# Optimization experiments

Hardware: AMD Instinct MI355X
Metric: run time of the kernel (lower is better)

Reference implementation:

```python
import jax, jax.numpy as jnp
import numpy as np

N_NODES = 50000
N_EDGES = 800000
IN_CH = 64
OUT_CH = 32
HEADS = 4
NUM_EDGE_TYPES = 64


def _sincos_pe(max_len, d_model):
    pos = np.arange(max_len, dtype=np.float32)[:, None]
    div = np.exp(np.arange(0, d_model, 2, dtype=np.float32) * (-np.log(10000.0) / d_model))
    pe = np.zeros((max_len, d_model), dtype=np.float32)
    pe[:, 0::2] = np.sin(pos * div)
    pe[:, 1::2] = np.cos(pos * div)
    return jnp.asarray(pe)


def setup_inputs() -> dict:
    key = jax.random.key(0)
    k1, k2, k3, k4, k5, k6 = jax.random.split(key, 6)
    x = jax.random.uniform(k1, (N_NODES, IN_CH), dtype=jnp.float32)
    edge_index = jax.random.randint(k2, (2, N_EDGES), 0, N_NODES, dtype=jnp.int64)
    edge_type = jax.random.randint(k3, (N_EDGES,), 0, NUM_EDGE_TYPES, dtype=jnp.int64)
    pe = _sincos_pe(NUM_EDGE_TYPES, IN_CH)
    W = jax.random.normal(k4, (IN_CH, HEADS * OUT_CH), dtype=jnp.float32) * 0.1
    att_src = jax.random.normal(k5, (HEADS, OUT_CH), dtype=jnp.float32) * 0.1
    att_dst = jax.random.normal(k6, (HEADS, OUT_CH), dtype=jnp.float32) * 0.1
    bias = jnp.zeros((HEADS * OUT_CH,), dtype=jnp.float32)
    return {"x": x, "edge_index": edge_index, "edge_type": edge_type, "pe": pe,
            "W": W, "att_src": att_src, "att_dst": att_dst, "bias": bias}


def reference(x, edge_index, edge_type, pe, W, att_src, att_dst, bias):
    N = x.shape[0]
    H, C = att_src.shape
    src, dst = edge_index[0], edge_index[1]

    # edge-wise positional encoding scatter-added into source nodes
    x_pos = x.at[src].add(pe[edge_type])

    # GATConv (PyG defaults: add_self_loops=True, negative_slope=0.2, concat=True)
    xl = (x_pos @ W).reshape(N, H, C)              # [N, H, C]
    a_src = (xl * att_src[None]).sum(-1)           # [N, H]
    a_dst = (xl * att_dst[None]).sum(-1)           # [N, H]

    self_idx = jnp.arange(N)
    src2 = jnp.concatenate([src, self_idx])        # [E'] with self loops
    dst2 = jnp.concatenate([dst, self_idx])

    alpha = jax.nn.leaky_relu(a_src[src2] + a_dst[dst2], 0.2)   # [E', H]
    amax = jax.ops.segment_max(alpha, dst2, num_segments=N)     # per-target max
    ex = jnp.exp(alpha - amax[dst2])
    denom = jax.ops.segment_sum(ex, dst2, num_segments=N)
    coef = ex / denom[dst2]                                     # segment softmax

    out = jax.ops.segment_sum(coef[:, :, None] * xl[src2], dst2, num_segments=N)
    out = out.reshape(N, H * C) + bias
    return jax.nn.elu(out)
```

## Files before the change

### kernel.cpp

```cpp
#include <hip/hip_runtime.h>
#include <cstdint>
#include <cstddef>

#define N_NODES 50000
#define N_EDGES 800000
#define IN_CH   64
#define OC      128
#define HEADS   4
#define CH      32

#define NB      391
#define BCAP    2560
#define EPB     2048
#define HIST_BLOCKS ((N_EDGES + EPB - 1) / EPB)

#define SENTINEL N_NODES

typedef __attribute__((ext_vector_type(8))) short short8;
typedef __attribute__((ext_vector_type(4))) float f32x4;

static inline int ceil_div(int a, int b){ return (a + b - 1) / b; }

__device__ __forceinline__ float lrelu(float x){ return fmaxf(x, 0.2f * x); }

__device__ __forceinline__ unsigned pack_bf16(float x, float y){
  unsigned ux = __float_as_uint(x), uy = __float_as_uint(y);
  ux += 0x7FFFu + ((ux >> 16) & 1u);
  uy += 0x7FFFu + ((uy >> 16) & 1u);
  return (ux >> 16) | (uy & 0xFFFF0000u);
}

__global__ __launch_bounds__(256) void k_histA(const int* __restrict__ ei,
                                               const int* __restrict__ et,
                                               int* __restrict__ btail,
                                               unsigned* __restrict__ bbuf){
  __shared__ int cnt[2 * NB + 2];
  __shared__ int pos[2 * NB + 2];
  int tid = threadIdx.x;
  for (int i = tid; i < 2 * NB + 2; i += 256) cnt[i] = 0;
  __syncthreads();

  int e0 = blockIdx.x * EPB;
  unsigned ed[8], es[8];
  #pragma unroll
  for (int j = 0; j < 8; ++j){
    int e = e0 + j * 256 + tid;
    ed[j] = 0xFFFFFFFFu; es[j] = 0xFFFFFFFFu;
    if (e < N_EDGES){
      int s = ei[e], d = ei[N_EDGES + e], t = et[e];
      ed[j] = ((unsigned)(d >> 7) << 23) | ((unsigned)(d & 127) << 16) | (unsigned)s;
      es[j] = ((unsigned)(s >> 7) << 23) | ((unsigned)(s & 127) << 16) | (unsigned)t;
      atomicAdd(&cnt[ed[j] >> 23], 1);
      atomicAdd(&cnt[NB + (es[j] >> 23)], 1);
    }
  }
  __syncthreads();
  for (int i = tid; i < 2 * NB; i += 256){
    int c = cnt[i];
    pos[i] = c ? atomicAdd(&btail[i], c) : 0;
  }
  __syncthreads();
  #pragma unroll
  for (int j = 0; j < 8; ++j){
    if (ed[j] != 0xFFFFFFFFu){
      int b = ed[j] >> 23;
      int p = atomicAdd(&pos[b], 1);
      if (p < BCAP) bbuf[(size_t)b * BCAP + p] = ed[j];
      int b2 = NB + (es[j] >> 23);
      int p2 = atomicAdd(&pos[b2], 1);
      if (p2 < BCAP) bbuf[(size_t)b2 * BCAP + p2] = es[j];
    }
  }
}

__global__ __launch_bounds__(256) void k_passB(const unsigned* __restrict__ bbuf,
                                               const int* __restrict__ btail,
                                               int* __restrict__ row_dst,
                                               unsigned short* __restrict__ lst,
                                               unsigned* __restrict__ cb){
  int g = blockIdx.x, tid = threadIdx.x;
  if (g < NB){
    __shared__ int cnt[128], sc[128], cur[128], red[256];
    __shared__ int sbase;
    int d0 = g << 7;
    int nn = min(128, N_NODES - d0);
    int cnt_b = min(btail[g], BCAP);
    int part = 0;
    for (int q = tid; q < g; q += 256) part += min(btail[q], BCAP);
    red[tid] = part; __syncthreads();
    for (int off = 128; off > 0; off >>= 1){
      if (tid < off) red[tid] += red[tid + off];
      __syncthreads();
    }
    if (tid == 0) sbase = red[0];
    if (tid < 128) cnt[tid] = 0;
    __syncthreads();
    int base0 = sbase;
    for (int i = tid; i < cnt_b; i += 256)
      atomicAdd(&cnt[(bbuf[(size_t)g * BCAP + i] >> 16) & 127], 1);
    __syncthreads();
    if (tid < 128) sc[tid] = cnt[tid];
    __syncthreads();
    for (int off = 1; off < 128; off <<= 1){
      int t = (tid < 128 && tid >= off) ? sc[tid - off] : 0;
      __syncthreads();
      if (tid < 128) sc[tid] += t;
      __syncthreads();
    }
    if (tid < nn){
      int ex = sc[tid] - cnt[tid];
      cur[tid] = ex;
      row_dst[d0 + tid] = base0 + ex;
    }
    if (g == NB - 1 && tid == 0) row_dst[N_NODES] = base0 + cnt_b;
    __syncthreads();
    for (int i = tid; i < cnt_b; i += 256){
      unsigned e = bbuf[(size_t)g * BCAP + i];
      int p = atomicAdd(&cur[(e >> 16) & 127], 1);
      lst[base0 + p] = (unsigned short)(e & 0xFFFFu);
    }
  } else {
    __shared__ unsigned hist[128 * 16];
    int n0 = (g - NB) << 7;
    int nn = min(128, N_NODES - n0);
    for (int i = tid; i < 2048; i += 256) hist[i] = 0;
    __syncthreads();
    int cnt_b = min(btail[g], BCAP);
    for (int i = tid; i < cnt_b; i += 256){
      unsigned e = bbuf[(size_t)g * BCAP + i];
      unsigned t = e & 63u;
      atomicAdd(&hist[((e >> 16) & 127) * 16 + (t >> 2)], 1u << (8 * (t & 3)));
    }
    __syncthreads();
    for (int o = tid; o < 4096; o += 256){
      int i = o >> 5, j = o & 31;
      if (i < nn){
        unsigned w = hist[i * 16 + (j >> 1)];
        unsigned sh = 16 * (j & 1);
        cb[(size_t)(n0 + i) * 32 + j] =
          pack_bf16((float)((w >> sh) & 0xFFu), (float)((w >> (sh + 8)) & 0xFFu));
      }
    }
  }
}

__global__ __launch_bounds__(256) void k_prep(const float* __restrict__ pe,
                                              const float* __restrict__ W,
                                              unsigned* __restrict__ Bh,
                                              int* __restrict__ btail,
                                              float* __restrict__ a_src,
                                              unsigned* __restrict__ xh,
                                              unsigned short* __restrict__ lst){
  __shared__ float sPe[64 * 64];
  __shared__ float sW64[64 * 16];
  __shared__ float sPeW[64 * 16];
  int tid = threadIdx.x;
  int nt = blockIdx.x;
  int n0 = nt * 16;
  if (nt == 0){
    for (int i = tid; i < 1024; i += 256) btail[i] = 0;
    if (tid < 64) xh[(size_t)SENTINEL * 64 + tid] = 0;
    if (tid < 4)  a_src[SENTINEL * 4 + tid] = -1e30f;
    if (tid < 8)  lst[N_EDGES + tid] = (unsigned short)SENTINEL;
  }
  for (int i = tid; i < 1024; i += 256)
    ((float4*)sPe)[i] = ((const float4*)pe)[i];
  for (int i = tid; i < 1024; i += 256){
    int k = i >> 4, j = i & 15;
    sW64[i] = W[k * 128 + n0 + j];
  }
  __syncthreads();
  for (int i = tid; i < 1024; i += 256){
    int t = i >> 4, j = i & 15;
    float a = 0.f;
    #pragma unroll
    for (int k = 0; k < 64; ++k) a += sPe[t * 64 + k] * sW64[k * 16 + j];
    sPeW[i] = a;
  }
  __syncthreads();
  for (int m = tid; m < 1024; m += 256){
    int j2 = m & 3, l = (m >> 2) & 63, kk = m >> 8;
    int k = kk * 32 + (l >> 4) * 8 + 2 * j2;
    int jl = l & 15;
    float v0, v1;
    if (k < 64){ v0 = sW64[k * 16 + jl]; v1 = sW64[(k + 1) * 16 + jl]; }
    else       { v0 = sPeW[(k - 64) * 16 + jl]; v1 = sPeW[(k - 63) * 16 + jl]; }
    Bh[nt * 1024 + m] = pack_bf16(v0, v1);
  }
}

#define GEMM_ROWS 64
__global__ __launch_bounds__(256) void k_gemm_mfma(const float* __restrict__ x,
                                                   const unsigned* __restrict__ cb,
                                                   const unsigned* __restrict__ Bh,
                                                   const float* __restrict__ att_s,
                                                   const float* __restrict__ att_d,
                                                   float* __restrict__ a_src,
                                                   float* __restrict__ a_dst,
                                                   unsigned* __restrict__ xh){
  __shared__ unsigned sA[4096];
  __shared__ unsigned sB[8192];
  int tid = threadIdx.x;
  int row0 = blockIdx.x * GEMM_ROWS;

  {
    const uint4* srcp = (const uint4*)Bh;
    uint4* dstp = (uint4*)sB;
    #pragma unroll
    for (int i = 0; i < 8; ++i) dstp[tid + i * 256] = srcp[tid + i * 256];
  }
  {
    int r = tid >> 2, q = tid & 3;
    int n = row0 + r;
    unsigned swz = (unsigned)((r & 7) << 4);
    float4 xv[4];
    if (n < N_NODES){
      const float4* xr = (const float4*)(x + (size_t)n * 64);
      #pragma unroll
      for (int i = 0; i < 4; ++i) xv[i] = xr[q * 4 + i];
    } else {
      #pragma unroll
      for (int i = 0; i < 4; ++i) xv[i] = make_float4(0.f, 0.f, 0.f, 0.f);
    }
    unsigned pk[8];
    #pragma unroll
    for (int i = 0; i < 4; ++i){
      pk[2 * i]     = pack_bf16(xv[i].x, xv[i].y);
      pk[2 * i + 1] = pack_bf16(xv[i].z, xv[i].w);
    }
    unsigned b0 = (unsigned)(r * 256 + q * 32);
    *(uint4*)(sA + (((b0)      ^ swz) >> 2)) = make_uint4(pk[0], pk[1], pk[2], pk[3]);
    *(uint4*)(sA + (((b0 + 16) ^ swz) >> 2)) = make_uint4(pk[4], pk[5], pk[6], pk[7]);
    uint4 c0, c1;
    if (n < N_NODES){
      const uint4* cr = (const uint4*)(cb + (size_t)n * 32);
      c0 = cr[q * 2]; c1 = cr[q * 2 + 1];
    } else {
      c0 = make_uint4(0, 0, 0, 0); c1 = c0;
    }
    unsigned b1 = (unsigned)(r * 256 + 128 + q * 32);
    *(uint4*)(sA + (((b1)      ^ swz) >> 2)) = c0;
    *(uint4*)(sA + (((b1 + 16) ^ swz) >> 2)) = c1;
  }
  __syncthreads();

  int wid = tid >> 6, l = tid & 63;
  int c15 = l & 15, kq = l >> 4;
  int arow = wid * 16 + c15;
  f32x4 acc[8];
  #pragma unroll
  for (int nt = 0; nt < 8; ++nt) acc[nt] = (f32x4){0.f, 0.f, 0.f, 0.f};

  #pragma unroll
  for (int kk = 0; kk < 4; ++kk){
    unsigned abyte = (unsigned)(arow * 256 + kk * 64 + kq * 16);
    abyte ^= (unsigned)((arow & 7) << 4);
    short8 af = *(const short8*)((const char*)sA + abyte);
    #pragma unroll
    for (int nt = 0; nt < 8; ++nt){
      short8 bf = *(const short8*)(sB + (size_t)((nt * 4 + kk) * 64 + l) * 4);
      acc[nt] = __builtin_amdgcn_mfma_f32_16x16x32_bf16(af, bf, acc[nt], 0, 0, 0);
    }
  }

  float asv[8], adv[8];
  #pragma unroll
  for (int nt = 0; nt < 8; ++nt){
    asv[nt] = att_s[nt * 16 + c15];
    adv[nt] = att_d[nt * 16 + c15];
  }
  #pragma unroll
  for (int r = 0; r < 4; ++r){
    int row = row0 + wid * 16 + kq * 4 + r;
    bool valid = row < N_NODES;
    #pragma unroll
    for (int h = 0; h < 4; ++h){
      float ps = acc[2 * h][r] * asv[2 * h] + acc[2 * h + 1][r] * asv[2 * h + 1];
      float pd = acc[2 * h][r] * adv[2 * h] + acc[2 * h + 1][r] * adv[2 * h + 1];
      #pragma unroll
      for (int m = 1; m < 16; m <<= 1){
        ps += __shfl_xor(ps, m);
        pd += __shfl_xor(pd, m);
      }
      if (valid && c15 == 0){
        a_src[row * 4 + h] = ps;
        a_dst[row * 4 + h] = pd;
      }
    }
    #pragma unroll
    for (int nt = 0; nt < 8; ++nt){
      float own = acc[nt][r];
      float nb = __shfl_xor(own, 1);
      if (valid && !(c15 & 1))
        xh[(size_t)row * 64 + nt * 8 + (c15 >> 1)] = pack_bf16(own, nb);
    }
  }
}

__global__ __launch_bounds__(256) void k_aggregate(const int* __restrict__ row_dst,
                                                   const unsigned short* __restrict__ lst,
                                                   const float* __restrict__ a_src,
                                                   const float* __restrict__ a_dst,
                                                   const unsigned* __restrict__ xh,
                                                   const float* __restrict__ bias,
                                                   float* __restrict__ out){
  int n = (blockIdx.x * blockDim.x + threadIdx.x) >> 6;
  if (n >= N_NODES) return;
  int l = threadIdx.x & 63;
  int h = l >> 4;
  float ad = a_dst[n * 4 + h];

  float w = __expf(lrelu(a_src[n * 4 + h] + ad));
  unsigned uv = xh[(size_t)n * 64 + l];
  float l0 = w, l1 = 0.f, l2 = 0.f, l3 = 0.f;
  float a0x = w * __uint_as_float(uv << 16);
  float a0y = w * __uint_as_float(uv & 0xFFFF0000u);
  float a1x = 0.f, a1y = 0.f, a2x = 0.f, a2y = 0.f, a3x = 0.f, a3y = 0.f;

  int k0 = row_dst[n], k1 = row_dst[n + 1];

  int sA = (int)lst[k0], sB = (int)lst[k0 + 1], sC = (int)lst[k0 + 2], sD = (int)lst[k0 + 3];
  unsigned uA = xh[(size_t)sA * 64 + l]; float bA = a_src[sA * 4 + h];
  unsigned uB = xh[(size_t)sB * 64 + l]; float bB = a_src[sB * 4 + h];
  unsigned uC = xh[(size_t)sC * 64 + l]; float bC = a_src[sC * 4 + h];
  unsigned uD = xh[(size_t)sD * 64 + l]; float bD = a_src[sD * 4 + h];

  for (int j = k0; j < k1; j += 4){
    int nsA = (int)lst[j + 4], nsB = (int)lst[j + 5];
    int nsC = (int)lst[j + 6], nsD = (int)lst[j + 7];
    unsigned nuA = xh[(size_t)nsA * 64 + l]; float nbA = a_src[nsA * 4 + h];
    unsigned nuB = xh[(size_t)nsB * 64 + l]; float nbB = a_src[nsB * 4 + h];
    unsigned nuC = xh[(size_t)nsC * 64 + l]; float nbC = a_src[nsC * 4 + h];
    unsigned nuD = xh[(size_t)nsD * 64 + l]; float nbD = a_src[nsD * 4 + h];
    float wA = __expf(lrelu(bA + ad));
    l0 += wA;
    a0x = fmaf(wA, __uint_as_float(uA << 16), a0x);
    a0y = fmaf(wA, __uint_as_float(uA & 0xFFFF0000u), a0y);
    float wB = (j + 1 < k1) ? __expf(lrelu(bB + ad)) : 0.f;
    l1 += wB;
    a1x = fmaf(wB, __uint_as_float(uB << 16), a1x);
    a1y = fmaf(wB, __uint_as_float(uB & 0xFFFF0000u), a1y);
    float wC = (j + 2 < k1) ? __expf(lrelu(bC + ad)) : 0.f;
    l2 += wC;
    a2x = fmaf(wC, __uint_as_float(uC << 16), a2x);
    a2y = fmaf(wC, __uint_as_float(uC & 0xFFFF0000u), a2y);
    float wD = (j + 3 < k1) ? __expf(lrelu(bD + ad)) : 0.f;
    l3 += wD;
    a3x = fmaf(wD, __uint_as_float(uD << 16), a3x);
    a3y = fmaf(wD, __uint_as_float(uD & 0xFFFF0000u), a3y);
    sA = nsA; uA = nuA; bA = nbA;
    sB = nsB; uB = nuB; bB = nbB;
    sC = nsC; uC = nuC; bC = nbC;
    sD = nsD; uD = nuD; bD = nbD;
  }
  float lsum = (l0 + l1) + (l2 + l3);
  float accx = (a0x + a1x) + (a2x + a3x);
  float accy = (a0y + a1y) + (a2y + a3y);
  float2 b = ((const float2*)bias)[l];
  float r0 = accx / lsum + b.x;
  float r1 = accy / lsum + b.y;
  float2 o;
  o.x = r0 > 0.f ? r0 : expm1f(r0);
  o.y = r1 > 0.f ? r1 : expm1f(r1);
  ((float2*)out)[(size_t)n * 64 + l] = o;
}

extern "C" void kernel_launch(void* const* d_in, const int* in_sizes, int n_in,
                              void* d_out, int out_size, void* d_ws, size_t ws_size,
                              hipStream_t stream){
  const float* x     = (const float*)d_in[0];
  const int*   ei    = (const int*)d_in[1];
  const int*   et    = (const int*)d_in[2];
  const float* pe    = (const float*)d_in[3];
  const float* W     = (const float*)d_in[4];
  const float* att_s = (const float*)d_in[5];
  const float* att_d = (const float*)d_in[6];
  const float* bias  = (const float*)d_in[7];
  float* out = (float*)d_out;

  int*      btail   = (int*)d_ws;
  int*      row_dst = btail + 1024;
  unsigned* Bh      = (unsigned*)(row_dst + N_NODES + 8);
  unsigned* cb      = Bh + 8192;
  float*    a_src   = (float*)(cb + (size_t)N_NODES * 32);
  float*    a_dst   = a_src + (size_t)(N_NODES + 1) * 4;
  unsigned* xh      = (unsigned*)(a_dst + (size_t)N_NODES * 4);
  unsigned* bbuf    = xh + (size_t)(N_NODES + 1) * 64;
  unsigned short* lst = (unsigned short*)(bbuf + (size_t)2 * NB * BCAP);

  const int B = 256;

  k_prep<<<8, B, 0, stream>>>(pe, W, Bh, btail, a_src, xh, lst);
  k_histA<<<HIST_BLOCKS, B, 0, stream>>>(ei, et, btail, bbuf);
  k_passB<<<2 * NB, B, 0, stream>>>(bbuf, btail, row_dst, lst, cb);
  k_gemm_mfma<<<ceil_div(N_NODES, GEMM_ROWS), B, 0, stream>>>(x, cb, Bh,
                                                              att_s, att_d,
                                                              a_src, a_dst, xh);
  k_aggregate<<<ceil_div(N_NODES * 64, B), B, 0, stream>>>(row_dst, lst, a_src, a_dst,
                                                           xh, bias, out);
}
```

Baseline: 109.0 us.

## Split wavefront into four edge slots with 16-byte feature loads in aggregation

```diff
diff --git a/kernel.cpp b/kernel.cpp
--- a/kernel.cpp
+++ b/kernel.cpp
@@ -22,6 +22,9 @@
 static inline int ceil_div(int a, int b){ return (a + b - 1) / b; }
 
 __device__ __forceinline__ float lrelu(float x){ return fmaxf(x, 0.2f * x); }
+
+__device__ __forceinline__ float bf_lo(unsigned u){ return __uint_as_float(u << 16); }
+__device__ __forceinline__ float bf_hi(unsigned u){ return __uint_as_float(u & 0xFFFF0000u); }
 
 __device__ __forceinline__ unsigned pack_bf16(float x, float y){
   unsigned ux = __float_as_uint(x), uy = __float_as_uint(y);
@@ -307,62 +310,65 @@
   int n = (blockIdx.x * blockDim.x + threadIdx.x) >> 6;
   if (n >= N_NODES) return;
   int l = threadIdx.x & 63;
-  int h = l >> 4;
+  int slot = l >> 4;
+  int q = l & 15;
+  int h = q >> 2;
   float ad = a_dst[n * 4 + h];
 
-  float w = __expf(lrelu(a_src[n * 4 + h] + ad));
-  unsigned uv = xh[(size_t)n * 64 + l];
-  float l0 = w, l1 = 0.f, l2 = 0.f, l3 = 0.f;
-  float a0x = w * __uint_as_float(uv << 16);
-  float a0y = w * __uint_as_float(uv & 0xFFFF0000u);
-  float a1x = 0.f, a1y = 0.f, a2x = 0.f, a2y = 0.f, a3x = 0.f, a3y = 0.f;
+  const uint4* xh4 = (const uint4*)xh;
+
+  uint4 sv = xh4[(size_t)n * 16 + q];
+  float wself = __expf(lrelu(a_src[n * 4 + h] + ad));
+  float sw = (slot == 0) ? wself : 0.f;
+  float lp = sw;
+  float acc[8];
+  acc[0] = sw * bf_lo(sv.x); acc[1] = sw * bf_hi(sv.x);
+  acc[2] = sw * bf_lo(sv.y); acc[3] = sw * bf_hi(sv.y);
+  acc[4] = sw * bf_lo(sv.z); acc[5] = sw * bf_hi(sv.z);
+  acc[6] = sw * bf_lo(sv.w); acc[7] = sw * bf_hi(sv.w);
 
   int k0 = row_dst[n], k1 = row_dst[n + 1];
 
-  int sA = (int)lst[k0], sB = (int)lst[k0 + 1], sC = (int)lst[k0 + 2], sD = (int)lst[k0 + 3];
-  unsigned uA = xh[(size_t)sA * 64 + l]; float bA = a_src[sA * 4 + h];
-  unsigned uB = xh[(size_t)sB * 64 + l]; float bB = a_src[sB * 4 + h];
-  unsigned uC = xh[(size_t)sC * 64 + l]; float bC = a_src[sC * 4 + h];
-  unsigned uD = xh[(size_t)sD * 64 + l]; float bD = a_src[sD * 4 + h];
+  int s = (int)lst[k0 + slot];
+  uint4 v = xh4[(size_t)s * 16 + q];
+  float b = a_src[s * 4 + h];
 
   for (int j = k0; j < k1; j += 4){
-    int nsA = (int)lst[j + 4], nsB = (int)lst[j + 5];
-    int nsC = (int)lst[j + 6], nsD = (int)lst[j + 7];
-    unsigned nuA = xh[(size_t)nsA * 64 + l]; float nbA = a_src[nsA * 4 + h];
-    unsigned nuB = xh[(size_t)nsB * 64 + l]; float nbB = a_src[nsB * 4 + h];
-    unsigned nuC = xh[(size_t)nsC * 64 + l]; float nbC = a_src[nsC * 4 + h];
-    unsigned nuD = xh[(size_t)nsD * 64 + l]; float nbD = a_src[nsD * 4 + h];
-    float wA = __expf(lrelu(bA + ad));
-    l0 += wA;
-    a0x = fmaf(wA, __uint_as_float(uA << 16), a0x);
-    a0y = fmaf(wA, __uint_as_float(uA & 0xFFFF0000u), a0y);
-    float wB = (j + 1 < k1) ? __expf(lrelu(bB + ad)) : 0.f;
-    l1 += wB;
-    a1x = fmaf(wB, __uint_as_float(uB << 16), a1x);
-    a1y = fmaf(wB, __uint_as_float(uB & 0xFFFF0000u), a1y);
-    float wC = (j + 2 < k1) ? __expf(lrelu(bC + ad)) : 0.f;
-    l2 += wC;
-    a2x = fmaf(wC, __uint_as_float(uC << 16), a2x);
-    a2y = fmaf(wC, __uint_as_float(uC & 0xFFFF0000u), a2y);
-    float wD = (j + 3 < k1) ? __expf(lrelu(bD + ad)) : 0.f;
-    l3 += wD;
-    a3x = fmaf(wD, __uint_as_float(uD << 16), a3x);
-    a3y = fmaf(wD, __uint_as_float(uD & 0xFFFF0000u), a3y);
-    sA = nsA; uA = nuA; bA = nbA;
-    sB = nsB; uB = nuB; bB = nbB;
-    sC = nsC; uC = nuC; bC = nbC;
-    sD = nsD; uD = nuD; bD = nbD;
-  }
-  float lsum = (l0 + l1) + (l2 + l3);
-  float accx = (a0x + a1x) + (a2x + a3x);
-  float accy = (a0y + a1y) + (a2y + a3y);
-  float2 b = ((const float2*)bias)[l];
-  float r0 = accx / lsum + b.x;
-  float r1 = accy / lsum + b.y;
-  float2 o;
-  o.x = r0 > 0.f ? r0 : expm1f(r0);
-  o.y = r1 > 0.f ? r1 : expm1f(r1);
-  ((float2*)out)[(size_t)n * 64 + l] = o;
+    int s2 = (int)lst[j + 4 + slot];
+    uint4 v2 = xh4[(size_t)s2 * 16 + q];
+    float b2 = a_src[s2 * 4 + h];
+    float w = (j + slot < k1) ? __expf(lrelu(b + ad)) : 0.f;
+    lp += w;
+    acc[0] = fmaf(w, bf_lo(v.x), acc[0]); acc[1] = fmaf(w, bf_hi(v.x), acc[1]);
+    acc[2] = fmaf(w, bf_lo(v.y), acc[2]); acc[3] = fmaf(w, bf_hi(v.y), acc[3]);
+    acc[4] = fmaf(w, bf_lo(v.z), acc[4]); acc[5] = fmaf(w, bf_hi(v.z), acc[5]);
+    acc[6] = fmaf(w, bf_lo(v.w), acc[6]); acc[7] = fmaf(w, bf_hi(v.w), acc[7]);
+    v = v2; b = b2; s = s2;
+  }
+
+  lp += __shfl_xor(lp, 16); lp += __shfl_xor(lp, 32);
+  #pragma unroll
+  for (int i = 0; i < 8; ++i){
+    acc[i] += __shfl_xor(acc[i], 16);
+    acc[i] += __shfl_xor(acc[i], 32);
+  }
+
+  if (slot == 0){
+    float inv = 1.f / lp;
+    const float* bq = bias + q * 8;
+    float4 o0, o1;
+    float r;
+    r = acc[0] * inv + bq[0]; o0.x = r > 0.f ? r : expm1f(r);
+    r = acc[1] * inv + bq[1]; o0.y = r > 0.f ? r : expm1f(r);
+    r = acc[2] * inv + bq[2]; o0.z = r > 0.f ? r : expm1f(r);
+    r = acc[3] * inv + bq[3]; o0.w = r > 0.f ? r : expm1f(r);
+    r = acc[4] * inv + bq[4]; o1.x = r > 0.f ? r : expm1f(r);
+    r = acc[5] * inv + bq[5]; o1.y = r > 0.f ? r : expm1f(r);
+    r = acc[6] * inv + bq[6]; o1.z = r > 0.f ? r : expm1f(r);
+    r = acc[7] * inv + bq[7]; o1.w = r > 0.f ? r : expm1f(r);
+    float4* op = (float4*)(out + (size_t)n * 128 + q * 8);
+    op[0] = o0; op[1] = o1;
+  }
 }
 
 extern "C" void kernel_launch(void* const* d_in, const int* in_sizes, int n_in,
```

Result: slower. 120.4 us (+10.5%).

## Stage bucket scatter in LDS and pad CSR rows with sentinels

Applied to the files above, without the earlier changes.

```diff
diff --git a/kernel.cpp b/kernel.cpp
--- a/kernel.cpp
+++ b/kernel.cpp
@@ -15,6 +15,7 @@
 #define HIST_BLOCKS ((N_EDGES + EPB - 1) / EPB)
 
 #define SENTINEL N_NODES
+#define LST_LEN  (N_EDGES + 4 * N_NODES)
 
 typedef __attribute__((ext_vector_type(8))) short short8;
 typedef __attribute__((ext_vector_type(4))) float f32x4;
@@ -22,6 +23,9 @@
 static inline int ceil_div(int a, int b){ return (a + b - 1) / b; }
 
 __device__ __forceinline__ float lrelu(float x){ return fmaxf(x, 0.2f * x); }
+
+__device__ __forceinline__ float bf_lo(unsigned u){ return __uint_as_float(u << 16); }
+__device__ __forceinline__ float bf_hi(unsigned u){ return __uint_as_float(u & 0xFFFF0000u); }
 
 __device__ __forceinline__ unsigned pack_bf16(float x, float y){
   unsigned ux = __float_as_uint(x), uy = __float_as_uint(y);
@@ -34,42 +38,76 @@
                                                const int* __restrict__ et,
                                                int* __restrict__ btail,
                                                unsigned* __restrict__ bbuf){
-  __shared__ int cnt[2 * NB + 2];
-  __shared__ int pos[2 * NB + 2];
+  __shared__ int cnt[784];
+  __shared__ int lofs[784];
+  __shared__ int gpos[784];
+  __shared__ unsigned stage[2 * EPB];
+  __shared__ int sred[256];
   int tid = threadIdx.x;
-  for (int i = tid; i < 2 * NB + 2; i += 256) cnt[i] = 0;
+  for (int i = tid; i < 784; i += 256) cnt[i] = 0;
   __syncthreads();
 
   int e0 = blockIdx.x * EPB;
-  unsigned ed[8], es[8];
+  unsigned ent[16];
+  int rnk[16];
+  short bck[16];
   #pragma unroll
   for (int j = 0; j < 8; ++j){
     int e = e0 + j * 256 + tid;
-    ed[j] = 0xFFFFFFFFu; es[j] = 0xFFFFFFFFu;
+    bck[2 * j] = -1; bck[2 * j + 1] = -1;
     if (e < N_EDGES){
       int s = ei[e], d = ei[N_EDGES + e], t = et[e];
-      ed[j] = ((unsigned)(d >> 7) << 23) | ((unsigned)(d & 127) << 16) | (unsigned)s;
-      es[j] = ((unsigned)(s >> 7) << 23) | ((unsigned)(s & 127) << 16) | (unsigned)t;
-      atomicAdd(&cnt[ed[j] >> 23], 1);
-      atomicAdd(&cnt[NB + (es[j] >> 23)], 1);
-    }
-  }
-  __syncthreads();
-  for (int i = tid; i < 2 * NB; i += 256){
-    int c = cnt[i];
-    pos[i] = c ? atomicAdd(&btail[i], c) : 0;
-  }
-  __syncthreads();
-  #pragma unroll
-  for (int j = 0; j < 8; ++j){
-    if (ed[j] != 0xFFFFFFFFu){
-      int b = ed[j] >> 23;
-      int p = atomicAdd(&pos[b], 1);
-      if (p < BCAP) bbuf[(size_t)b * BCAP + p] = ed[j];
-      int b2 = NB + (es[j] >> 23);
-      int p2 = atomicAdd(&pos[b2], 1);
-      if (p2 < BCAP) bbuf[(size_t)b2 * BCAP + p2] = es[j];
-    }
+      int bd = d >> 7, bs = s >> 7;
+      ent[2 * j]     = ((unsigned)bd << 23) | ((unsigned)(d & 127) << 16) | (unsigned)s;
+      ent[2 * j + 1] = ((unsigned)bs << 23) | ((unsigned)(s & 127) << 16) | (unsigned)t;
+      bck[2 * j]     = (short)bd;
+      bck[2 * j + 1] = (short)(391 + bs);
+      rnk[2 * j]     = atomicAdd(&cnt[bd], 1);
+      rnk[2 * j + 1] = atomicAdd(&cnt[391 + bs], 1);
+    }
+  }
+  __syncthreads();
+
+  int v[4], pre[4], run = 0;
+  #pragma unroll
+  for (int i = 0; i < 4; ++i){
+    int idx = tid * 4 + i;
+    v[i] = (idx < 784) ? cnt[idx] : 0;
+    pre[i] = run; run += v[i];
+  }
+  sred[tid] = run; __syncthreads();
+  for (int off = 1; off < 256; off <<= 1){
+    int t = (tid >= off) ? sred[tid - off] : 0;
+    __syncthreads();
+    sred[tid] += t;
+    __syncthreads();
+  }
+  int toff = sred[tid] - run;
+  #pragma unroll
+  for (int i = 0; i < 4; ++i){
+    int idx = tid * 4 + i;
+    if (idx < 784) lofs[idx] = toff + pre[i];
+  }
+  __syncthreads();
+
+  #pragma unroll
+  for (int j = 0; j < 16; ++j){
+    if (bck[j] >= 0) stage[lofs[bck[j]] + rnk[j]] = ent[j];
+  }
+  for (int b = tid; b < 782; b += 256){
+    int c = cnt[b];
+    gpos[b] = c ? atomicAdd(&btail[b], c) : 0;
+  }
+  __syncthreads();
+
+  int totalD = lofs[391];
+  int totalA = lofs[782];
+  for (int i = tid; i < totalA; i += 256){
+    unsigned e = stage[i];
+    int b9 = (int)(e >> 23);
+    int bc = (i < totalD) ? b9 : 391 + b9;
+    int gp = gpos[bc] + (i - lofs[bc]);
+    if (gp < BCAP) bbuf[(size_t)bc * BCAP + gp] = e;
   }
 }
 
@@ -95,7 +133,7 @@
     if (tid == 0) sbase = red[0];
     if (tid < 128) cnt[tid] = 0;
     __syncthreads();
-    int base0 = sbase;
+    int base0 = sbase + 4 * d0;
     for (int i = tid; i < cnt_b; i += 256)
       atomicAdd(&cnt[(bbuf[(size_t)g * BCAP + i] >> 16) & 127], 1);
     __syncthreads();
@@ -109,15 +147,21 @@
     }
     if (tid < nn){
       int ex = sc[tid] - cnt[tid];
-      cur[tid] = ex;
-      row_dst[d0 + tid] = base0 + ex;
-    }
-    if (g == NB - 1 && tid == 0) row_dst[N_NODES] = base0 + cnt_b;
+      cur[tid] = ex + 4 * tid;
+      row_dst[d0 + tid] = base0 + ex + 4 * tid;
+    }
+    if (g == NB - 1 && tid == 0) row_dst[N_NODES] = base0 + cnt_b + 4 * nn;
     __syncthreads();
     for (int i = tid; i < cnt_b; i += 256){
       unsigned e = bbuf[(size_t)g * BCAP + i];
       int p = atomicAdd(&cur[(e >> 16) & 127], 1);
       lst[base0 + p] = (unsigned short)(e & 0xFFFFu);
+    }
+    __syncthreads();
+    if (tid < nn){
+      int pe_ = cur[tid];
+      #pragma unroll
+      for (int k = 0; k < 4; ++k) lst[base0 + pe_ + k] = (unsigned short)SENTINEL;
     }
   } else {
     __shared__ unsigned hist[128 * 16];
@@ -161,7 +205,7 @@
     for (int i = tid; i < 1024; i += 256) btail[i] = 0;
     if (tid < 64) xh[(size_t)SENTINEL * 64 + tid] = 0;
     if (tid < 4)  a_src[SENTINEL * 4 + tid] = -1e30f;
-    if (tid < 8)  lst[N_EDGES + tid] = (unsigned short)SENTINEL;
+    if (tid < 32) lst[LST_LEN + tid] = (unsigned short)SENTINEL;
   }
   for (int i = tid; i < 1024; i += 256)
     ((float4*)sPe)[i] = ((const float4*)pe)[i];
@@ -313,11 +357,11 @@
   float w = __expf(lrelu(a_src[n * 4 + h] + ad));
   unsigned uv = xh[(size_t)n * 64 + l];
   float l0 = w, l1 = 0.f, l2 = 0.f, l3 = 0.f;
-  float a0x = w * __uint_as_float(uv << 16);
-  float a0y = w * __uint_as_float(uv & 0xFFFF0000u);
+  float a0x = w * bf_lo(uv), a0y = w * bf_hi(uv);
   float a1x = 0.f, a1y = 0.f, a2x = 0.f, a2y = 0.f, a3x = 0.f, a3y = 0.f;
 
-  int k0 = row_dst[n], k1 = row_dst[n + 1];
+  int k0 = row_dst[n];
+  int k1 = row_dst[n + 1] - 4;
 
   int sA = (int)lst[k0], sB = (int)lst[k0 + 1], sC = (int)lst[k0 + 2], sD = (int)lst[k0 + 3];
   unsigned uA = xh[(size_t)sA * 64 + l]; float bA = a_src[sA * 4 + h];
@@ -334,24 +378,18 @@
     unsigned nuD = xh[(size_t)nsD * 64 + l]; float nbD = a_src[nsD * 4 + h];
     float wA = __expf(lrelu(bA + ad));
     l0 += wA;
-    a0x = fmaf(wA, __uint_as_float(uA << 16), a0x);
-    a0y = fmaf(wA, __uint_as_float(uA & 0xFFFF0000u), a0y);
-    float wB = (j + 1 < k1) ? __expf(lrelu(bB + ad)) : 0.f;
+    a0x = fmaf(wA, bf_lo(uA), a0x); a0y = fmaf(wA, bf_hi(uA), a0y);
+    float wB = __expf(lrelu(bB + ad));
     l1 += wB;
-    a1x = fmaf(wB, __uint_as_float(uB << 16), a1x);
-    a1y = fmaf(wB, __uint_as_float(uB & 0xFFFF0000u), a1y);
-    float wC = (j + 2 < k1) ? __expf(lrelu(bC + ad)) : 0.f;
+    a1x = fmaf(wB, bf_lo(uB), a1x); a1y = fmaf(wB, bf_hi(uB), a1y);
+    float wC = __expf(lrelu(bC + ad));
     l2 += wC;
-    a2x = fmaf(wC, __uint_as_float(uC << 16), a2x);
-    a2y = fmaf(wC, __uint_as_float(uC & 0xFFFF0000u), a2y);
-    float wD = (j + 3 < k1) ? __expf(lrelu(bD + ad)) : 0.f;
+    a2x = fmaf(wC, bf_lo(uC), a2x); a2y = fmaf(wC, bf_hi(uC), a2y);
+    float wD = __expf(lrelu(bD + ad));
     l3 += wD;
-    a3x = fmaf(wD, __uint_as_float(uD << 16), a3x);
-    a3y = fmaf(wD, __uint_as_float(uD & 0xFFFF0000u), a3y);
-    sA = nsA; uA = nuA; bA = nbA;
-    sB = nsB; uB = nuB; bB = nbB;
-    sC = nsC; uC = nuC; bC = nbC;
-    sD = nsD; uD = nuD; bD = nbD;
+    a3x = fmaf(wD, bf_lo(uD), a3x); a3y = fmaf(wD, bf_hi(uD), a3y);
+    uA = nuA; bA = nbA; uB = nuB; bB = nbB;
+    uC = nuC; bC = nbC; uD = nuD; bD = nbD;
   }
   float lsum = (l0 + l1) + (l2 + l3);
   float accx = (a0x + a1x) + (a2x + a3x);
```

Result: faster. 105.5 us (-3.2%).
